# Kernel optimization log

Hardware: AMD Instinct MI355X
Metric: run time of the kernel (lower is better)

Reference implementation:

```python
import jax, jax.numpy as jnp
import numpy as np

N = 16777216  # number of trajectory points

def setup_inputs() -> dict:
    key = jax.random.key(0)
    k1, k2, k3 = jax.random.split(key, 3)
    traj_pred = jax.random.normal(k1, (N + 1,), dtype=jnp.float32)
    traj_true_x = jax.random.normal(k2, (N,), dtype=jnp.float32)
    traj_true_y = jax.random.normal(k3, (N,), dtype=jnp.float32)
    return {"traj_pred": traj_pred, "traj_true_x": traj_true_x, "traj_true_y": traj_true_y}

def reference(traj_pred, traj_true_x, traj_true_y):
    # Faithful vectorization of:
    #   diffs += (x[i] - pred[i])**2 + (y[i] - pred[i+1])**2  for i in range(N)
    pred = traj_pred.reshape(-1)
    n = traj_true_x.shape[0]
    dx = traj_true_x - pred[:n]
    dy = traj_true_y - pred[1:n + 1]
    return jnp.sum(dx * dx + dy * dy)
```

## Files before the change

kernel.cpp:

```cpp
#include <hip/hip_runtime.h>


typedef float fx4 __attribute__((ext_vector_type(4)));

__global__ void TrajLoss_zero_kernel(float* out) {
    if (threadIdx.x == 0 && blockIdx.x == 0) out[0] = 0.0f;
}

__global__ __launch_bounds__(256) void TrajLoss_6141803233879_kernel(
    const float* __restrict__ pred,
    const float* __restrict__ x,
    const float* __restrict__ y,
    float* __restrict__ out,
    int n4,
    int n)
{
    const int tid    = blockIdx.x * blockDim.x + threadIdx.x;
    const int stride = gridDim.x * blockDim.x;

    float a0 = 0.0f, a1 = 0.0f, a2 = 0.0f, a3 = 0.0f;
    const fx4* x4 = (const fx4*)x;
    const fx4* p4 = (const fx4*)pred;

    int i = tid;

    if (tid == 0) {
        float dx, dy;
        dx = x[0] - pred[0];                       a0 += dx*dx;
        dx = x[1] - pred[1]; dy = y[0] - pred[1];  a1 += dx*dx + dy*dy;
        dx = x[2] - pred[2]; dy = y[1] - pred[2];  a2 += dx*dx + dy*dy;
        dx = x[3] - pred[3]; dy = y[2] - pred[3];  a3 += dx*dx + dy*dy;
        if ((n & 3) == 0) {
            dy = y[n - 1] - pred[n];               a0 += dy*dy;
        } else {
            dy = y[(n4 << 2) - 1] - pred[n4 << 2]; a0 += dy*dy;
            for (int j = n4 << 2; j < n; ++j) {
                dx = x[j] - pred[j];
                dy = y[j] - pred[j + 1];
                a0 += dx*dx + dy*dy;
            }
        }
        i += stride;
    }

    #pragma unroll 16
    for (; i < n4; i += stride) {
        fx4 xv = __builtin_nontemporal_load(x4 + i);
        fx4 pa = __builtin_nontemporal_load(p4 + i);
        fx4 yb = __builtin_nontemporal_load((const fx4*)(y + (i << 2) - 1));
        float dx, dy;
        dx = xv.x - pa.x; dy = yb.x - pa.x; a0 += dx*dx + dy*dy;
        dx = xv.y - pa.y; dy = yb.y - pa.y; a1 += dx*dx + dy*dy;
        dx = xv.z - pa.z; dy = yb.z - pa.z; a2 += dx*dx + dy*dy;
        dx = xv.w - pa.w; dy = yb.w - pa.w; a3 += dx*dx + dy*dy;
    }

    float acc = (a0 + a1) + (a2 + a3);

    #pragma unroll
    for (int off = 32; off > 0; off >>= 1)
        acc += __shfl_down(acc, off, 64);

    __shared__ float smem[4];
    const int lane = threadIdx.x & 63;
    const int wave = threadIdx.x >> 6;
    if (lane == 0) smem[wave] = acc;
    __syncthreads();

    if (threadIdx.x == 0) {
        float s = smem[0] + smem[1] + smem[2] + smem[3];
        atomicAdd(out, s);
    }
}

extern "C" void kernel_launch(void* const* d_in, const int* in_sizes, int n_in,
                              void* d_out, int out_size, void* d_ws, size_t ws_size,
                              hipStream_t stream) {
    const float* pred = (const float*)d_in[0];
    const float* x    = (const float*)d_in[1];
    const float* y    = (const float*)d_in[2];
    float* out = (float*)d_out;

    const int n  = in_sizes[1];
    const int n4 = n >> 2;

    TrajLoss_zero_kernel<<<1, 64, 0, stream>>>(out);

    const int block = 256;
    const int grid = 1024;
    TrajLoss_6141803233879_kernel<<<grid, block, 0, stream>>>(pred, x, y, out, n4, n);
}
```

Before: 183.0 us.

## Use aligned y loads with wave shuffle and a fully unrolled fast path

Adds a specialised kernel for the exact size where n4 equals 16 grid strides. It loads y with aligned float4 loads and gets the shifted element from the neighbouring lane with a shuffle, with lane 0 reading the edge value separately. It also fully unrolls the 16 iterations with no loop bounds. The aim is to remove misaligned y loads and loop overhead, at the cost of extra shuffles, scattered edge loads, and a path that only runs for a size matching the launch configuration.

```diff
diff --git a/kernel.cpp b/kernel.cpp
--- a/kernel.cpp
+++ b/kernel.cpp
@@ -12,8 +12,72 @@
     const float* __restrict__ x,
     const float* __restrict__ y,
     float* __restrict__ out,
-    int n4,
     int n)
+{
+    const int tid    = blockIdx.x * blockDim.x + threadIdx.x;
+    const int stride = gridDim.x * blockDim.x;
+    const int lane   = threadIdx.x & 63;
+
+    float a0 = 0.0f, a1 = 0.0f, a2 = 0.0f, a3 = 0.0f;
+    const fx4* x4 = (const fx4*)x;
+    const fx4* p4 = (const fx4*)pred;
+    const fx4* y4 = (const fx4*)y;
+
+    if (tid == 0) {
+        float dN = y[n - 1] - pred[n];
+        a0 += dN * dN;
+    }
+
+    float edge[16];
+    if (lane == 0) {
+        #pragma unroll
+        for (int k = 0; k < 16; ++k) {
+            int idx = ((tid + k * stride) << 2) - 1;
+            edge[k] = y[idx < 0 ? 0 : idx];
+        }
+        if (tid == 0) edge[0] = pred[0];
+    }
+
+    #pragma unroll
+    for (int k = 0; k < 16; ++k) {
+        const int i = tid + k * stride;
+        fx4 xv = __builtin_nontemporal_load(x4 + i);
+        fx4 pa = __builtin_nontemporal_load(p4 + i);
+        fx4 yv = __builtin_nontemporal_load(y4 + i);
+
+        float ym1 = __shfl_up(yv.w, 1, 64);
+        ym1 = (lane == 0) ? edge[k] : ym1;
+
+        float dx, dy;
+        dx = xv.x - pa.x; dy = ym1  - pa.x; a0 += dx*dx + dy*dy;
+        dx = xv.y - pa.y; dy = yv.x - pa.y; a1 += dx*dx + dy*dy;
+        dx = xv.z - pa.z; dy = yv.y - pa.z; a2 += dx*dx + dy*dy;
+        dx = xv.w - pa.w; dy = yv.z - pa.w; a3 += dx*dx + dy*dy;
+    }
+
+    float acc = (a0 + a1) + (a2 + a3);
+
+    #pragma unroll
+    for (int off = 32; off > 0; off >>= 1)
+        acc += __shfl_down(acc, off, 64);
+
+    __shared__ float smem[4];
+    const int wave = threadIdx.x >> 6;
+    if (lane == 0) smem[wave] = acc;
+    __syncthreads();
+
+    if (threadIdx.x == 0) {
+        float s = smem[0] + smem[1] + smem[2] + smem[3];
+        atomicAdd(out, s);
+    }
+}
+
+__global__ __launch_bounds__(256) void TrajLoss_generic_kernel(
+    const float* __restrict__ pred,
+    const float* __restrict__ x,
+    const float* __restrict__ y,
+    float* __restrict__ out,
+    int n4, int n)
 {
     const int tid    = blockIdx.x * blockDim.x + threadIdx.x;
     const int stride = gridDim.x * blockDim.x;
@@ -87,6 +151,12 @@
     TrajLoss_zero_kernel<<<1, 64, 0, stream>>>(out);
 
     const int block = 256;
-    const int grid = 1024;
-    TrajLoss_6141803233879_kernel<<<grid, block, 0, stream>>>(pred, x, y, out, n4, n);
+    const int grid  = 1024;
+    const int stride = grid * block;
+
+    if ((n & 3) == 0 && n4 == 16 * stride) {
+        TrajLoss_6141803233879_kernel<<<grid, block, 0, stream>>>(pred, x, y, out, n);
+    } else {
+        TrajLoss_generic_kernel<<<grid, block, 0, stream>>>(pred, x, y, out, n4, n);
+    }
 }
```

Result: no change. 181.7 us, median of 2 (-0.7%).
